# Performance work log

Measured on AMD Instinct MI355X. Metric: run time of the kernel, lower is better.

The kernel has to match this reference:

```python
import jax, jax.numpy as jnp
import numpy as np

# --- module hyperparameters (from init_kwargs) ---
NUM_CHANNELS = 31
WINDOW_SIZE = 3
IN_DIM = 2 * WINDOW_SIZE + 1          # 7
GRID_SIZE = 5
SPLINE_ORDER = 3
GRID_RANGE = (-1.0, 1.0)
N_BASIS = GRID_SIZE + SPLINE_ORDER    # 8 spline coefficients per input dim
COEF_LEN = IN_DIM * 1 * N_BASIS       # 56
KAN_PARAMS = COEF_LEN + IN_DIM + IN_DIM  # 70 = coef + univariate_w + residual_w


def bspline_basis(x):
    """Cox-de Boor B-spline bases of order SPLINE_ORDER on a uniform grid.
    x: [...,] -> returns [..., N_BASIS]."""
    lo, hi = GRID_RANGE
    h = (hi - lo) / GRID_SIZE
    # extended knot vector: grid_size + 2*k + 1 knots
    knots = lo + h * jnp.arange(-SPLINE_ORDER, GRID_SIZE + SPLINE_ORDER + 1,
                                dtype=x.dtype)
    xe = x[..., None]
    b = ((xe >= knots[:-1]) & (xe < knots[1:])).astype(x.dtype)
    for p in range(1, SPLINE_ORDER + 1):
        left = (xe - knots[: -(p + 1)]) / (knots[p:-1] - knots[: -(p + 1)]) * b[..., :-1]
        right = (knots[p + 1:] - xe) / (knots[p + 1:] - knots[1:-p]) * b[..., 1:]
        b = left + right
    return b  # [..., N_BASIS]


def setup_inputs() -> dict:
    key = jax.random.key(0)
    k1, k2, k3 = jax.random.split(key, 3)
    B, C, D, H, W = 2, NUM_CHANNELS, IN_DIM, 192, 192
    windowed_x = jax.random.normal(k1, (B, C, D, H, W), dtype=jnp.float32)
    # hypernetwork generator: 3x3 conv  C -> KAN_PARAMS
    gen_w = jax.random.normal(k2, (KAN_PARAMS, C, 3, 3), dtype=jnp.float32) * 0.05
    gen_b = jax.random.normal(k3, (KAN_PARAMS,), dtype=jnp.float32) * 0.05
    return {"windowed_x": windowed_x, "gen_w": gen_w, "gen_b": gen_b}


def reference(windowed_x, gen_w, gen_b):
    B, C, D, H, W = windowed_x.shape
    # shared-params branch: global context -> per-pixel KAN weights
    ctx = windowed_x.mean(axis=2)  # [B, C, H, W]
    wts = jax.lax.conv_general_dilated(
        ctx, gen_w, window_strides=(1, 1), padding="SAME",
        dimension_numbers=("NCHW", "OIHW", "NCHW"))
    wts = wts + gen_b[None, :, None, None]            # [B, P, H, W]
    wts = jnp.moveaxis(wts, 1, -1)                    # [B, H, W, P]
    # unpack per-pixel KAN parameters (out_dim == 1 squeezed)
    coef = wts[..., :COEF_LEN].reshape(B, H, W, D, N_BASIS)   # [B,H,W,7,8]
    uw = wts[..., COEF_LEN:COEF_LEN + D]                      # [B,H,W,7]
    rw = wts[..., COEF_LEN + D:COEF_LEN + 2 * D]              # [B,H,W,7]
    # per-pixel, per-channel spline window evaluation (weights shared over C)
    x = jnp.moveaxis(windowed_x, 2, -1)               # [B, C, H, W, 7]
    basis = bspline_basis(x)                          # [B, C, H, W, 7, 8]
    spline = jnp.einsum("bchwdg,bhwdg,bhwd->bchw", basis, coef, uw)
    resid = jnp.einsum("bchwd,bhwd->bchw", jax.nn.silu(x), rw)
    return spline + resid                             # [B, C, H, W]
```

## Files before the change

kernel.cpp:

```cpp
#include <hip/hip_runtime.h>
#include <math.h>

#define NBATCH 2
#define NC 31
#define ND 7
#define NH 192
#define NW 192
#define HW (NH * NW)
#define NP (NBATCH * HW)
#define NBASIS 8
#define CLEN 56
#define KP 70

#define N4 (NBATCH * NC * (HW / 4))
#define GWB_N (9 * 80 * 32)

#define B_WORDS (3 * 66 * 32)
#define SMEM_BYTES (KP * 64 * 4)

#define KPX 64

typedef __attribute__((ext_vector_type(8))) short s16x8;
typedef __attribute__((ext_vector_type(4))) float f32x4;

__device__ __forceinline__ unsigned short f2bf(float f)
{
    unsigned u = __float_as_uint(f);
    u += 0x7FFFu + ((u >> 16) & 1u);
    return (unsigned short)(u >> 16);
}

__global__ __launch_bounds__(256) void ctx_mean_kernel(
    const float4* __restrict__ x4, float4* __restrict__ ctx4,
    const float* __restrict__ gw, unsigned short* __restrict__ gwb)
{
    const int HW4 = HW / 4;
    int idx = blockIdx.x * 256 + threadIdx.x;
    if (idx < N4) {
        int hw4 = idx % HW4;
        int bc  = idx / HW4;
        const float4* src = x4 + (size_t)bc * (ND * HW4) + hw4;
        float4 a = src[0];
#pragma unroll
        for (int d = 1; d < ND; ++d) {
            float4 v = src[d * HW4];
            a.x += v.x; a.y += v.y; a.z += v.z; a.w += v.w;
        }
        const float inv = 1.0f / 7.0f;
        a.x *= inv; a.y *= inv; a.z *= inv; a.w *= inv;
        ctx4[idx] = a;
        return;
    }
    int e = idx - N4;
    if (e < GWB_N) {
        int s  = e / 2560;
        int r  = e - s * 2560;
        int m  = r >> 5;
        int ic = r & 31;
        float v = (m < KP && ic < NC) ? gw[m * (NC * 9) + ic * 9 + s] : 0.f;
        gwb[e] = f2bf(v);
    }
}

__device__ __forceinline__ float spline_part(float xv, const float* cb, int d)
{
    float t = __builtin_fmaf(xv, 2.5f, 5.5f);
    float fi = floorf(t);
    int i = (int)fi;
    float u = t - fi;
    float u2 = u * u, u3 = u2 * u;
    float um = 1.f - u;
    float w0 = um * um * um * (1.f / 6.f);
    float w3 = u3 * (1.f / 6.f);
    float w1 = (3.f * u3 - 6.f * u2 + 4.f) * (1.f / 6.f);
    float w2 = 1.f - w0 - w1 - w3;
    int j0 = i - 3;
    float sd = 0.f;
#pragma unroll
    for (int k = 0; k < 4; ++k) {
        int j = j0 + k;
        bool valid = ((unsigned)j) < 8u;
        int jc = j & 7;
        float wk = (k == 0) ? w0 : (k == 1) ? w1 : (k == 2) ? w2 : w3;
        float cf = cb[(d * NBASIS + jc) * KPX];
        sd += (valid ? wk : 0.f) * cf;
    }
    return sd;
}

__device__ __forceinline__ float silu(float xv)
{
    return xv / (1.f + __expf(-xv));
}

__global__ __launch_bounds__(256, 4) void fused_kernel(
    const float* __restrict__ ctx, const unsigned short* __restrict__ gwb,
    const float* __restrict__ gb, const float* __restrict__ x,
    float* __restrict__ out)
{
    __shared__ __align__(16) unsigned char smem[SMEM_BYTES];
    unsigned short* Bt = (unsigned short*)smem;
    float* scoef = (float*)smem;

    const int tid  = threadIdx.x;
    const int lane = tid & 63;
    const int wv   = tid >> 6;
    const int gr   = blockIdx.x / 3;
    const int x0   = (blockIdx.x % 3) * 64;
    const int b    = gr / NH;
    const int y    = gr - b * NH;

    if (tid < 3 * 66) {
        int row = tid / 66;
        int col = tid - row * 66;
        int gy = y + row - 1, gx = x0 + col - 1;
        bool ok = (gy >= 0) && (gy < NH) && (gx >= 0) && (gx < NW);
        int cgy = ok ? gy : 0, cgx = ok ? gx : 0;
        const float* src = ctx + (size_t)(b * NC) * HW + cgy * NW + cgx;
        unsigned dw[16];
        if (ok) {
            float v[NC];
#pragma unroll
            for (int ic = 0; ic < NC; ++ic) v[ic] = src[(size_t)ic * HW];
#pragma unroll
            for (int j = 0; j < 16; ++j) {
                unsigned lo = f2bf(v[2 * j]);
                unsigned hi = (2 * j + 1 < NC) ? (unsigned)f2bf(v[2 * j + 1]) : 0u;
                dw[j] = lo | (hi << 16);
            }
        } else {
#pragma unroll
            for (int j = 0; j < 16; ++j) dw[j] = 0u;
        }
        uint4* dst = (uint4*)(Bt + tid * 32);
#pragma unroll
        for (int q = 0; q < 4; ++q)
            dst[q] = make_uint4(dw[4 * q], dw[4 * q + 1], dw[4 * q + 2], dw[4 * q + 3]);
    }

    const int hw = y * NW + x0 + lane;
    const float* xb = x + (size_t)(b * NC) * (ND * HW) + hw;
    const int c0 = wv * 8;
    float cur[2][ND];
    {
        int ca = min(c0, 30), cb2 = min(c0 + 1, 30);
#pragma unroll
        for (int d = 0; d < ND; ++d) {
            cur[0][d] = xb[((size_t)ca * ND + d) * HW];
            cur[1][d] = xb[((size_t)cb2 * ND + d) * HW];
        }
    }
    __syncthreads();

    const int lm = lane & 15;
    const int kb = lane >> 4;

    f32x4 acc[5];
#pragma unroll
    for (int mt = 0; mt < 5; ++mt)
#pragma unroll
        for (int j = 0; j < 4; ++j) {
            int m = mt * 16 + kb * 4 + j;
            acc[mt][j] = (m < KP) ? gb[m] : 0.f;
        }

    const unsigned short* ap = gwb + lm * 32 + kb * 8;
    const unsigned short* bp = Bt + (wv * 16 + lm) * 32 + kb * 8;

#pragma unroll
    for (int s = 0; s < 9; ++s) {
        const int dy = s / 3, dx = s % 3;
        s16x8 bf = *(const s16x8*)(bp + (dy * 66 + dx) * 32);
#pragma unroll
        for (int mt = 0; mt < 5; ++mt) {
            s16x8 af = *(const s16x8*)(ap + (s * 80 + mt * 16) * 32);
            acc[mt] = __builtin_amdgcn_mfma_f32_16x16x32_bf16(af, bf, acc[mt], 0, 0, 0);
        }
    }
    __syncthreads();

    {
        const int px = wv * 16 + lm;
#pragma unroll
        for (int mt = 0; mt < 5; ++mt)
#pragma unroll
            for (int j = 0; j < 4; ++j) {
                int m = mt * 16 + kb * 4 + j;
                if (m < KP) scoef[m * KPX + px] = acc[mt][j];
            }
    }
    __syncthreads();

    const float* cbl = scoef + lane;

    float uw[ND], rw[ND];
#pragma unroll
    for (int d = 0; d < ND; ++d) {
        uw[d] = cbl[(CLEN + d) * KPX];
        rw[d] = cbl[(CLEN + ND + d) * KPX];
    }

    float* ob = out + (b * NC) * HW + hw;

    float nxt[2][ND];
#pragma unroll
    for (int pr = 0; pr < 4; ++pr) {
        int ca = min(c0 + 2 * pr, 30), cb2 = min(c0 + 2 * pr + 1, 30);
        if (pr < 3) {
            int na = min(c0 + 2 * pr + 2, 30), nb = min(c0 + 2 * pr + 3, 30);
#pragma unroll
            for (int d = 0; d < ND; ++d) {
                nxt[0][d] = xb[((size_t)na * ND + d) * HW];
                nxt[1][d] = xb[((size_t)nb * ND + d) * HW];
            }
        }
        float sa = 0.f, sb = 0.f;
#pragma unroll
        for (int d = 0; d < ND; ++d) {
            sa += uw[d] * spline_part(cur[0][d], cbl, d) + rw[d] * silu(cur[0][d]);
            sb += uw[d] * spline_part(cur[1][d], cbl, d) + rw[d] * silu(cur[1][d]);
        }
        ob[(size_t)ca * HW] = sa;
        ob[(size_t)cb2 * HW] = sb;
        if (pr < 3) {
#pragma unroll
            for (int d = 0; d < ND; ++d) {
                cur[0][d] = nxt[0][d];
                cur[1][d] = nxt[1][d];
            }
        }
    }
}

extern "C" void kernel_launch(void* const* d_in, const int* in_sizes, int n_in,
                              void* d_out, int out_size, void* d_ws, size_t ws_size,
                              hipStream_t stream)
{
    const float* x  = (const float*)d_in[0];
    const float* gw = (const float*)d_in[1];
    const float* gb = (const float*)d_in[2];
    float* out = (float*)d_out;

    float* ctx = (float*)d_ws;
    unsigned short* gwb = (unsigned short*)(ctx + (size_t)NBATCH * NC * HW);

    ctx_mean_kernel<<<dim3(N4 / 256 + (GWB_N + 255) / 256), 256, 0, stream>>>(
        (const float4*)x, (float4*)ctx, gw, gwb);
    fused_kernel<<<dim3(NP / 64), 256, 0, stream>>>(ctx, gwb, gb, x, out);
}
```

Baseline: 135.2 us.

## Split channels across two grid rows and pad spline coefficients for branchless lookup

The fused kernel now launches a second grid dimension so each block processes only four channels per wave (the upper half overlaps on channel 27), doubling the block count while each block recomputes the 3x3 conv hypernetwork. Spline coefficients are stored in shared memory with zero-padded rows so the four-tap B-spline lookup uses a clamped index without per-tap validity selects. The aim is more parallelism and a shorter per-thread serial channel loop plus fewer ALU ops per spline, at the cost of duplicating the MFMA weight generation and the ctx loads across two blocks.

```diff
diff --git a/kernel.cpp b/kernel.cpp
--- a/kernel.cpp
+++ b/kernel.cpp
@@ -15,10 +15,9 @@
 #define N4 (NBATCH * NC * (HW / 4))
 #define GWB_N (9 * 80 * 32)
 
+#define SROWS 126
+#define SMEM_BYTES (SROWS * 64 * 4)
 #define B_WORDS (3 * 66 * 32)
-#define SMEM_BYTES (KP * 64 * 4)
-
-#define KPX 64
 
 typedef __attribute__((ext_vector_type(8))) short s16x8;
 typedef __attribute__((ext_vector_type(4))) float f32x4;
@@ -62,30 +61,21 @@
     }
 }
 
-__device__ __forceinline__ float spline_part(float xv, const float* cb, int d)
+__device__ __forceinline__ float spline2(float xv, const float* cbl, int d)
 {
     float t = __builtin_fmaf(xv, 2.5f, 5.5f);
     float fi = floorf(t);
+    float u = t - fi;
     int i = (int)fi;
-    float u = t - fi;
+    i = min(max(i, -1), 11);
     float u2 = u * u, u3 = u2 * u;
     float um = 1.f - u;
     float w0 = um * um * um * (1.f / 6.f);
     float w3 = u3 * (1.f / 6.f);
     float w1 = (3.f * u3 - 6.f * u2 + 4.f) * (1.f / 6.f);
     float w2 = 1.f - w0 - w1 - w3;
-    int j0 = i - 3;
-    float sd = 0.f;
-#pragma unroll
-    for (int k = 0; k < 4; ++k) {
-        int j = j0 + k;
-        bool valid = ((unsigned)j) < 8u;
-        int jc = j & 7;
-        float wk = (k == 0) ? w0 : (k == 1) ? w1 : (k == 2) ? w2 : w3;
-        float cf = cb[(d * NBASIS + jc) * KPX];
-        sd += (valid ? wk : 0.f) * cf;
-    }
-    return sd;
+    const float* p = cbl + (d * 16 + 1 + i) * 64;
+    return w0 * p[0] + w1 * p[64] + w2 * p[128] + w3 * p[192];
 }
 
 __device__ __forceinline__ float silu(float xv)
@@ -138,17 +128,15 @@
             dst[q] = make_uint4(dw[4 * q], dw[4 * q + 1], dw[4 * q + 2], dw[4 * q + 3]);
     }
 
+    const int c0 = (blockIdx.y == 0) ? wv * 4
+                                     : ((wv == 3) ? 27 : 16 + wv * 4);
     const int hw = y * NW + x0 + lane;
     const float* xb = x + (size_t)(b * NC) * (ND * HW) + hw;
-    const int c0 = wv * 8;
     float cur[2][ND];
-    {
-        int ca = min(c0, 30), cb2 = min(c0 + 1, 30);
-#pragma unroll
-        for (int d = 0; d < ND; ++d) {
-            cur[0][d] = xb[((size_t)ca * ND + d) * HW];
-            cur[1][d] = xb[((size_t)cb2 * ND + d) * HW];
-        }
+#pragma unroll
+    for (int d = 0; d < ND; ++d) {
+        cur[0][d] = xb[((size_t)c0 * ND + d) * HW];
+        cur[1][d] = xb[((size_t)(c0 + 1) * ND + d) * HW];
     }
     __syncthreads();
 
@@ -179,6 +167,12 @@
     }
     __syncthreads();
 
+    for (int f = tid; f < 56 * 64; f += 256) {
+        int r  = f >> 6, px = f & 63;
+        int d  = r >> 3, o = r & 7;
+        int row = d * 16 + (o < 4 ? o : o + 8);
+        scoef[row * 64 + px] = 0.f;
+    }
     {
         const int px = wv * 16 + lm;
 #pragma unroll
@@ -186,7 +180,11 @@
 #pragma unroll
             for (int j = 0; j < 4; ++j) {
                 int m = mt * 16 + kb * 4 + j;
-                if (m < KP) scoef[m * KPX + px] = acc[mt][j];
+                if (m < KP) {
+                    int row = (m < CLEN) ? ((m >> 3) << 4) + 4 + (m & 7)
+                                         : 56 + m;
+                    scoef[row * 64 + px] = acc[mt][j];
+                }
             }
     }
     __syncthreads();
@@ -196,33 +194,32 @@
     float uw[ND], rw[ND];
 #pragma unroll
     for (int d = 0; d < ND; ++d) {
-        uw[d] = cbl[(CLEN + d) * KPX];
-        rw[d] = cbl[(CLEN + ND + d) * KPX];
+        uw[d] = cbl[(112 + d) * 64];
+        rw[d] = cbl[(119 + d) * 64];
     }
 
     float* ob = out + (b * NC) * HW + hw;
 
     float nxt[2][ND];
 #pragma unroll
-    for (int pr = 0; pr < 4; ++pr) {
-        int ca = min(c0 + 2 * pr, 30), cb2 = min(c0 + 2 * pr + 1, 30);
-        if (pr < 3) {
-            int na = min(c0 + 2 * pr + 2, 30), nb = min(c0 + 2 * pr + 3, 30);
+    for (int pr = 0; pr < 2; ++pr) {
+        int ca = c0 + 2 * pr, cb2 = ca + 1;
+        if (pr == 0) {
 #pragma unroll
             for (int d = 0; d < ND; ++d) {
-                nxt[0][d] = xb[((size_t)na * ND + d) * HW];
-                nxt[1][d] = xb[((size_t)nb * ND + d) * HW];
+                nxt[0][d] = xb[((size_t)(c0 + 2) * ND + d) * HW];
+                nxt[1][d] = xb[((size_t)(c0 + 3) * ND + d) * HW];
             }
         }
         float sa = 0.f, sb = 0.f;
 #pragma unroll
         for (int d = 0; d < ND; ++d) {
-            sa += uw[d] * spline_part(cur[0][d], cbl, d) + rw[d] * silu(cur[0][d]);
-            sb += uw[d] * spline_part(cur[1][d], cbl, d) + rw[d] * silu(cur[1][d]);
+            sa += uw[d] * spline2(cur[0][d], cbl, d) + rw[d] * silu(cur[0][d]);
+            sb += uw[d] * spline2(cur[1][d], cbl, d) + rw[d] * silu(cur[1][d]);
         }
         ob[(size_t)ca * HW] = sa;
         ob[(size_t)cb2 * HW] = sb;
-        if (pr < 3) {
+        if (pr == 0) {
 #pragma unroll
             for (int d = 0; d < ND; ++d) {
                 cur[0][d] = nxt[0][d];
@@ -246,5 +243,5 @@
 
     ctx_mean_kernel<<<dim3(N4 / 256 + (GWB_N + 255) / 256), 256, 0, stream>>>(
         (const float4*)x, (float4*)ctx, gw, gwb);
-    fused_kernel<<<dim3(NP / 64), 256, 0, stream>>>(ctx, gwb, gb, x, out);
-}
+    fused_kernel<<<dim3(NP / 64, 2), 256, 0, stream>>>(ctx, gwb, gb, x, out);
+}
```

After: 144.8 us. 1.07x slower.

## Fuse channel-mean context computation into the fused hypernetwork kernel

Applied to the files above, without the earlier changes.

Removes the separate context-mean pass and its global intermediate buffer, and computes the 7-way mean over the window dimension directly while staging the 3x66 halo tile for the conv GEMM. The first kernel now only converts generator weights to bf16. This saves a full write and reread of the context tensor but re-reads the input about three times per pixel through the halo, with many serial strided loads per thread in the prologue.

```diff
diff --git a/kernel.cpp b/kernel.cpp
--- a/kernel.cpp
+++ b/kernel.cpp
@@ -12,11 +12,10 @@
 #define CLEN 56
 #define KP 70
 
-#define N4 (NBATCH * NC * (HW / 4))
 #define GWB_N (9 * 80 * 32)
 
+#define SMEM_BYTES (KP * 64 * 4)
 #define B_WORDS (3 * 66 * 32)
-#define SMEM_BYTES (KP * 64 * 4)
 
 #define KPX 64
 
@@ -30,28 +29,10 @@
     return (unsigned short)(u >> 16);
 }
 
-__global__ __launch_bounds__(256) void ctx_mean_kernel(
-    const float4* __restrict__ x4, float4* __restrict__ ctx4,
+__global__ __launch_bounds__(256) void gwb_kernel(
     const float* __restrict__ gw, unsigned short* __restrict__ gwb)
 {
-    const int HW4 = HW / 4;
-    int idx = blockIdx.x * 256 + threadIdx.x;
-    if (idx < N4) {
-        int hw4 = idx % HW4;
-        int bc  = idx / HW4;
-        const float4* src = x4 + (size_t)bc * (ND * HW4) + hw4;
-        float4 a = src[0];
-#pragma unroll
-        for (int d = 1; d < ND; ++d) {
-            float4 v = src[d * HW4];
-            a.x += v.x; a.y += v.y; a.z += v.z; a.w += v.w;
-        }
-        const float inv = 1.0f / 7.0f;
-        a.x *= inv; a.y *= inv; a.z *= inv; a.w *= inv;
-        ctx4[idx] = a;
-        return;
-    }
-    int e = idx - N4;
+    int e = blockIdx.x * 256 + threadIdx.x;
     if (e < GWB_N) {
         int s  = e / 2560;
         int r  = e - s * 2560;
@@ -94,9 +75,8 @@
 }
 
 __global__ __launch_bounds__(256, 4) void fused_kernel(
-    const float* __restrict__ ctx, const unsigned short* __restrict__ gwb,
-    const float* __restrict__ gb, const float* __restrict__ x,
-    float* __restrict__ out)
+    const unsigned short* __restrict__ gwb, const float* __restrict__ gb,
+    const float* __restrict__ x, float* __restrict__ out)
 {
     __shared__ __align__(16) unsigned char smem[SMEM_BYTES];
     unsigned short* Bt = (unsigned short*)smem;
@@ -116,12 +96,19 @@
         int gy = y + row - 1, gx = x0 + col - 1;
         bool ok = (gy >= 0) && (gy < NH) && (gx >= 0) && (gx < NW);
         int cgy = ok ? gy : 0, cgx = ok ? gx : 0;
-        const float* src = ctx + (size_t)(b * NC) * HW + cgy * NW + cgx;
+        const float* src = x + (size_t)(b * NC) * (ND * HW) + cgy * NW + cgx;
         unsigned dw[16];
         if (ok) {
+            const float inv7 = 1.0f / 7.0f;
             float v[NC];
 #pragma unroll
-            for (int ic = 0; ic < NC; ++ic) v[ic] = src[(size_t)ic * HW];
+            for (int ic = 0; ic < NC; ++ic) {
+                const float* sc = src + (size_t)ic * (ND * HW);
+                float s = sc[0];
+#pragma unroll
+                for (int d = 1; d < ND; ++d) s += sc[(size_t)d * HW];
+                v[ic] = s * inv7;
+            }
 #pragma unroll
             for (int j = 0; j < 16; ++j) {
                 unsigned lo = f2bf(v[2 * j]);
@@ -241,10 +228,8 @@
     const float* gb = (const float*)d_in[2];
     float* out = (float*)d_out;
 
-    float* ctx = (float*)d_ws;
-    unsigned short* gwb = (unsigned short*)(ctx + (size_t)NBATCH * NC * HW);
-
-    ctx_mean_kernel<<<dim3(N4 / 256 + (GWB_N + 255) / 256), 256, 0, stream>>>(
-        (const float4*)x, (float4*)ctx, gw, gwb);
-    fused_kernel<<<dim3(NP / 64), 256, 0, stream>>>(ctx, gwb, gb, x, out);
-}
+    unsigned short* gwb = (unsigned short*)d_ws;
+
+    gwb_kernel<<<dim3((GWB_N + 255) / 256), 256, 0, stream>>>(gw, gwb);
+    fused_kernel<<<dim3(NP / 64), 256, 0, stream>>>(gwb, gb, x, out);
+}
```

Result: slower. 182.8 us (+35.2%).
